# Optimization experiments

Measured on AMD Instinct MI355X. Metric: run time of the kernel, lower is better.

## Reference

```python
import jax, jax.numpy as jnp
import numpy as np

B, T, L, V, C = 4096, 200, 8, 64, 16
N_BERN = 32        # first 32 vars are bernoulli (sigmoid link), last 32 poisson (exp link)
LINPRED_MAX = 20.0


def setup_inputs() -> dict:
    key = jax.random.key(0)
    ks = jax.random.split(key, 6)
    return {
        "epsilon": jax.random.normal(ks[0], (B, T, L), dtype=jnp.float32),
        "u": jax.random.normal(ks[1], (B, 1, V), dtype=jnp.float32),
        "x": jax.random.normal(ks[2], (B, T, C), dtype=jnp.float32),
        # learned parameters (per VARGLLVM.__init__)
        "A": jax.random.normal(ks[3], (L, L), dtype=jnp.float32) * 0.1,
        "logvar_z1": jnp.zeros((L,), dtype=jnp.float32),
        "beta0": jnp.zeros((L,), dtype=jnp.float32),   # VAR1_intercept (frozen zeros)
        "beta1": jnp.zeros((L,), dtype=jnp.float32),   # VAR1_slope (frozen zeros)
        "intercepts": jnp.zeros((V,), dtype=jnp.float32),
        "wz": jax.random.normal(ks[4], (L, V), dtype=jnp.float32) * 0.1,
        "wx": jax.random.normal(ks[5], (C, V), dtype=jnp.float32) * 0.1,
        "logvar_u": jnp.zeros((V,), dtype=jnp.float32),
    }


def _var1(epsilon, A, logvar_z1, beta0, beta1):
    """z_1 = eps_1 * sqrt(exp(logvar_z1)); z_t = z_{t-1} @ A + beta0 + beta1*t + eps_t."""
    z0 = epsilon[:, 0, :] * jnp.exp(0.5 * logvar_z1)          # (B, L)
    eps_rest = jnp.swapaxes(epsilon[:, 1:, :], 0, 1)          # (T-1, B, L)
    ts = jnp.arange(1, epsilon.shape[1], dtype=epsilon.dtype)  # (T-1,)

    def step(z_prev, inp):
        eps_t, t = inp
        z_t = z_prev @ A + beta0 + beta1 * t + eps_t
        return z_t, z_t

    _, zs = jax.lax.scan(step, z0, (eps_rest, ts))            # (T-1, B, L)
    z = jnp.concatenate([z0[None], zs], axis=0)               # (T, B, L)
    return jnp.swapaxes(z, 0, 1)                              # (B, T, L)


def reference(epsilon, u, x, A, logvar_z1, beta0, beta1, intercepts, wz, wx, logvar_u):
    z = _var1(epsilon, A, logvar_z1, beta0, beta1)            # (B, T, L)
    linpar = (intercepts[None, None, :]
              + x @ wx                                        # (B, T, V)
              + z @ wz                                        # (B, T, V)
              + u * jnp.exp(0.5 * logvar_u)[None, None, :])   # broadcast (B, 1, V)
    linpar = jnp.clip(linpar, -LINPRED_MAX, LINPRED_MAX)
    is_bern = jnp.arange(V) < N_BERN                          # (V,) link selector
    condmean = jnp.where(is_bern, jax.nn.sigmoid(linpar), jnp.exp(linpar))
    return linpar, condmean
```

## Files before the change

kernel.cpp:

```cpp
#include <hip/hip_runtime.h>
#include <hip/hip_bf16.h>

#define BB 4096
#define TT 200
#define LL 8
#define VV 64
#define CC 16
#define NBERN 32
#define CLIP 20.0f
#define TC 25
#define NCH (TT / TC)
#define TOTW (BB * NCH)
#define WPB 4
#define LBLK (TOTW / WPB)
#define XF4 (TC * CC / 4)
#define ZF4 (TC * LL / 4)
#define BUF4T (XF4 + ZF4)
#define SEGT 25

__global__ __launch_bounds__(64) void var1_v4(
    const float* __restrict__ eps,
    const float* __restrict__ A,
    const float* __restrict__ logvar_z1,
    const float* __restrict__ beta0,
    const float* __restrict__ beta1,
    float* __restrict__ zout)
{
    const int tid = threadIdx.x;
    const int bl  = tid >> 3;
    const int s   = tid & 7;
    const int b   = blockIdx.x * 8 + bl;

    __shared__ float Mb[2][64];
    __shared__ float Pw8[64];
    __shared__ float P[64];
    __shared__ float zendS[8][8][8];
    __shared__ float initS[8][8][8];

    const int pi = tid >> 3, pj = tid & 7;
    Mb[0][tid] = A[pi * 8 + pj];
    __syncthreads();
    float v;
    v = 0.f;
#pragma unroll
    for (int l = 0; l < 8; ++l) v = fmaf(Mb[0][pi*8+l], Mb[0][l*8+pj], v);
    Mb[1][tid] = v; __syncthreads();
    v = 0.f;
#pragma unroll
    for (int l = 0; l < 8; ++l) v = fmaf(Mb[1][pi*8+l], Mb[1][l*8+pj], v);
    Mb[0][tid] = v; __syncthreads();
    v = 0.f;
#pragma unroll
    for (int l = 0; l < 8; ++l) v = fmaf(Mb[0][pi*8+l], Mb[0][l*8+pj], v);
    Mb[1][tid] = v; Pw8[tid] = v; __syncthreads();
    v = 0.f;
#pragma unroll
    for (int l = 0; l < 8; ++l) v = fmaf(Mb[1][pi*8+l], Mb[1][l*8+pj], v);
    Mb[0][tid] = v; __syncthreads();
    v = 0.f;
#pragma unroll
    for (int l = 0; l < 8; ++l) v = fmaf(Mb[0][pi*8+l], Pw8[l*8+pj], v);
    Mb[1][tid] = v; __syncthreads();
    v = 0.f;
#pragma unroll
    for (int l = 0; l < 8; ++l) v = fmaf(Mb[1][pi*8+l], A[l*8+pj], v);
    P[tid] = v; __syncthreads();

    float Am[8][8], B0[8], B1[8], SL[8];
#pragma unroll
    for (int l = 0; l < 8; ++l)
#pragma unroll
        for (int jj = 0; jj < 8; ++jj) Am[l][jj] = A[l * 8 + jj];
#pragma unroll
    for (int jj = 0; jj < 8; ++jj) {
        B0[jj] = beta0[jj];
        B1[jj] = beta1[jj];
        SL[jj] = __expf(0.5f * logvar_z1[jj]);
    }

    const float* myeps = eps + ((size_t)b * TT + s * SEGT) * LL;
    const int k0 = (s == 0) ? 1 : 0;

    float z[8];
#pragma unroll
    for (int jj = 0; jj < 8; ++jj) z[jj] = 0.f;
    if (s == 0) {
#pragma unroll
        for (int jj = 0; jj < 8; ++jj) z[jj] = myeps[jj] * SL[jj];
    }
#pragma unroll 5
    for (int k = k0; k < SEGT; ++k) {
        const int t = s * SEGT + k;
        const float4 e0 = *(const float4*)(myeps + k * 8);
        const float4 e1 = *(const float4*)(myeps + k * 8 + 4);
        const float ef[8] = {e0.x, e0.y, e0.z, e0.w, e1.x, e1.y, e1.z, e1.w};
        const float tf = (float)t;
        float zn[8];
#pragma unroll
        for (int jj = 0; jj < 8; ++jj) {
            float a = fmaf(B1[jj], tf, B0[jj]) + ef[jj];
#pragma unroll
            for (int l = 0; l < 8; ++l) a = fmaf(z[l], Am[l][jj], a);
            zn[jj] = a;
        }
#pragma unroll
        for (int jj = 0; jj < 8; ++jj) z[jj] = zn[jj];
    }
#pragma unroll
    for (int jj = 0; jj < 8; ++jj) zendS[bl][s][jj] = z[jj];
    __syncthreads();

    if (s == 0) {
        float E[8];
#pragma unroll
        for (int jj = 0; jj < 8; ++jj) E[jj] = zendS[bl][0][jj];
        for (int ss = 1; ss < 8; ++ss) {
#pragma unroll
            for (int jj = 0; jj < 8; ++jj) initS[bl][ss][jj] = E[jj];
            float En[8];
#pragma unroll
            for (int jj = 0; jj < 8; ++jj) {
                float c = 0.f;
#pragma unroll
                for (int l = 0; l < 8; ++l) c = fmaf(E[l], P[l * 8 + jj], c);
                En[jj] = zendS[bl][ss][jj] + c;
            }
#pragma unroll
            for (int jj = 0; jj < 8; ++jj) E[jj] = En[jj];
        }
    }
    __syncthreads();

    float* zb = zout + ((size_t)b * TT + s * SEGT) * LL;
    if (s == 0) {
#pragma unroll
        for (int jj = 0; jj < 8; ++jj) z[jj] = myeps[jj] * SL[jj];
        *(float4*)(zb)     = make_float4(z[0], z[1], z[2], z[3]);
        *(float4*)(zb + 4) = make_float4(z[4], z[5], z[6], z[7]);
    } else {
#pragma unroll
        for (int jj = 0; jj < 8; ++jj) z[jj] = initS[bl][s][jj];
    }
#pragma unroll 5
    for (int k = k0; k < SEGT; ++k) {
        const int t = s * SEGT + k;
        const float4 e0 = *(const float4*)(myeps + k * 8);
        const float4 e1 = *(const float4*)(myeps + k * 8 + 4);
        const float ef[8] = {e0.x, e0.y, e0.z, e0.w, e1.x, e1.y, e1.z, e1.w};
        const float tf = (float)t;
        float zn[8];
#pragma unroll
        for (int jj = 0; jj < 8; ++jj) {
            float a = fmaf(B1[jj], tf, B0[jj]) + ef[jj];
#pragma unroll
            for (int l = 0; l < 8; ++l) a = fmaf(z[l], Am[l][jj], a);
            zn[jj] = a;
        }
#pragma unroll
        for (int jj = 0; jj < 8; ++jj) z[jj] = zn[jj];
        *(float4*)(zb + (size_t)k * 8)     = make_float4(z[0], z[1], z[2], z[3]);
        *(float4*)(zb + (size_t)k * 8 + 4) = make_float4(z[4], z[5], z[6], z[7]);
    }
}

__global__ __launch_bounds__(256) void link_nt(
    const float* __restrict__ z,
    const float* __restrict__ u,
    const float* __restrict__ x,
    const float* __restrict__ intercepts,
    const float* __restrict__ wz,
    const float* __restrict__ wx,
    const float* __restrict__ logvar_u,
    float* __restrict__ lp_out,
    float* __restrict__ cm_out)
{
    const int w    = threadIdx.x >> 6;
    const int lane = threadIdx.x & 63;
    const int gw   = blockIdx.x * WPB + w;
    const int b    = gw >> 3;
    const int t0   = (gw & 7) * TC;
    const int v    = lane;

    __shared__ __align__(16) float4 buf[WPB][BUF4T];

    float wxv[CC];
#pragma unroll
    for (int c = 0; c < CC; ++c) wxv[c] = wx[c * VV + v];
    float wzv[LL];
#pragma unroll
    for (int l = 0; l < LL; ++l) wzv[l] = wz[l * VV + v];
    const float base = intercepts[v] + u[(size_t)b * VV + v] * __expf(0.5f * logvar_u[v]);

    const float4* gx4 = (const float4*)(x + ((size_t)b * TT + t0) * CC);
    const float4* gz4 = (const float4*)(z + ((size_t)b * TT + t0) * LL);
    float4* bw = buf[w];
    {
        const int i0 = lane;
        bw[i0] = (i0 < XF4) ? gx4[i0] : gz4[i0 - XF4];
        const int i1 = lane + 64;
        bw[i1] = (i1 < XF4) ? gx4[i1] : gz4[i1 - XF4];
        const int i2 = lane + 128;
        if (i2 < BUF4T) bw[i2] = gz4[i2 - XF4];
    }

    const float4* xs4 = bw;
    const float4* zs4 = bw + XF4;

    float* lp = lp_out + ((size_t)b * TT + t0) * VV + v;
    float* cm = cm_out + ((size_t)b * TT + t0) * VV + v;

    float4 cx0 = xs4[0], cx1 = xs4[1], cx2 = xs4[2], cx3 = xs4[3];
    float4 cz0 = zs4[0], cz1 = zs4[1];

    for (int tt = 0; tt < TC; ++tt) {
        float4 nx0, nx1, nx2, nx3, nz0, nz1;
        if (tt + 1 < TC) {
            nx0 = xs4[(tt + 1) * 4 + 0]; nx1 = xs4[(tt + 1) * 4 + 1];
            nx2 = xs4[(tt + 1) * 4 + 2]; nx3 = xs4[(tt + 1) * 4 + 3];
            nz0 = zs4[(tt + 1) * 2 + 0]; nz1 = zs4[(tt + 1) * 2 + 1];
        }

        float a0 = base, a1 = 0.f, a2 = 0.f, a3 = 0.f;
        a0 = fmaf(cx0.x, wxv[0],  a0); a0 = fmaf(cx0.y, wxv[1],  a0);
        a0 = fmaf(cx0.z, wxv[2],  a0); a0 = fmaf(cx0.w, wxv[3],  a0);
        a1 = fmaf(cx1.x, wxv[4],  a1); a1 = fmaf(cx1.y, wxv[5],  a1);
        a1 = fmaf(cx1.z, wxv[6],  a1); a1 = fmaf(cx1.w, wxv[7],  a1);
        a2 = fmaf(cx2.x, wxv[8],  a2); a2 = fmaf(cx2.y, wxv[9],  a2);
        a2 = fmaf(cx2.z, wxv[10], a2); a2 = fmaf(cx2.w, wxv[11], a2);
        a3 = fmaf(cx3.x, wxv[12], a3); a3 = fmaf(cx3.y, wxv[13], a3);
        a3 = fmaf(cx3.z, wxv[14], a3); a3 = fmaf(cx3.w, wxv[15], a3);
        a0 = fmaf(cz0.x, wzv[0],  a0); a0 = fmaf(cz0.y, wzv[1],  a0);
        a1 = fmaf(cz0.z, wzv[2],  a1); a1 = fmaf(cz0.w, wzv[3],  a1);
        a2 = fmaf(cz1.x, wzv[4],  a2); a2 = fmaf(cz1.y, wzv[5],  a2);
        a3 = fmaf(cz1.z, wzv[6],  a3); a3 = fmaf(cz1.w, wzv[7],  a3);

        float acc = (a0 + a1) + (a2 + a3);
        acc = fminf(fmaxf(acc, -CLIP), CLIP);
        const float cmv = (v < NBERN) ? (1.0f / (1.0f + __expf(-acc)))
                                      : __expf(acc);
        __builtin_nontemporal_store(acc, lp + (size_t)tt * VV);
        __builtin_nontemporal_store(cmv, cm + (size_t)tt * VV);

        cx0 = nx0; cx1 = nx1; cx2 = nx2; cx3 = nx3;
        cz0 = nz0; cz1 = nz1;
    }
}

__global__ __launch_bounds__(256) void vargllvm_fused(
    const float* __restrict__ eps, const float* __restrict__ u,
    const float* __restrict__ x, const float* __restrict__ A,
    const float* __restrict__ logvar_z1, const float* __restrict__ beta0,
    const float* __restrict__ beta1, const float* __restrict__ intercepts,
    const float* __restrict__ wz, const float* __restrict__ wx,
    const float* __restrict__ logvar_u,
    float* __restrict__ linpar_out, float* __restrict__ condmean_out)
{
    const int wave = threadIdx.x >> 6;
    const int lane = threadIdx.x & 63;
    const int b    = blockIdx.x * 4 + wave;
    const int v    = lane;

    float wxv[CC];
#pragma unroll
    for (int c = 0; c < CC; ++c) wxv[c] = wx[c * VV + v];
    float wzv[LL];
#pragma unroll
    for (int l = 0; l < LL; ++l) wzv[l] = wz[l * VV + v];
    const float base = intercepts[v] + u[(size_t)b * VV + v] * __expf(0.5f * logvar_u[v]);

    float Ar[LL][LL];
#pragma unroll
    for (int l = 0; l < LL; ++l)
#pragma unroll
        for (int j = 0; j < LL; ++j) Ar[l][j] = A[l * LL + j];
    float b0[LL], b1[LL];
#pragma unroll
    for (int j = 0; j < LL; ++j) { b0[j] = beta0[j]; b1[j] = beta1[j]; }

    const float* epsb = eps + (size_t)b * TT * LL;
    const float* xb   = x   + (size_t)b * TT * CC;
    float* lp = linpar_out   + (size_t)b * TT * VV + v;
    float* cm = condmean_out + (size_t)b * TT * VV + v;

    float zv[LL];
#pragma unroll
    for (int j = 0; j < LL; ++j) zv[j] = epsb[j] * __expf(0.5f * logvar_z1[j]);

    for (int t = 0; t < TT; ++t) {
        if (t > 0) {
            float zn[LL];
            const float tf = (float)t;
#pragma unroll
            for (int j = 0; j < LL; ++j) {
                float a = fmaf(b1[j], tf, b0[j]) + epsb[t * LL + j];
#pragma unroll
                for (int l = 0; l < LL; ++l) a = fmaf(zv[l], Ar[l][j], a);
                zn[j] = a;
            }
#pragma unroll
            for (int j = 0; j < LL; ++j) zv[j] = zn[j];
        }
        float acc = base;
#pragma unroll
        for (int c = 0; c < CC; ++c) acc = fmaf(xb[t * CC + c], wxv[c], acc);
#pragma unroll
        for (int l = 0; l < LL; ++l) acc = fmaf(zv[l], wzv[l], acc);
        acc = fminf(fmaxf(acc, -CLIP), CLIP);
        float cmv = (v < NBERN) ? (1.0f / (1.0f + __expf(-acc))) : __expf(acc);
        lp[(size_t)t * VV] = acc;
        cm[(size_t)t * VV] = cmv;
    }
}

extern "C" void kernel_launch(void* const* d_in, const int* in_sizes, int n_in,
                              void* d_out, int out_size, void* d_ws, size_t ws_size,
                              hipStream_t stream) {
    const float* eps        = (const float*)d_in[0];
    const float* u          = (const float*)d_in[1];
    const float* x          = (const float*)d_in[2];
    const float* A          = (const float*)d_in[3];
    const float* logvar_z1  = (const float*)d_in[4];
    const float* beta0      = (const float*)d_in[5];
    const float* beta1      = (const float*)d_in[6];
    const float* intercepts = (const float*)d_in[7];
    const float* wz         = (const float*)d_in[8];
    const float* wx         = (const float*)d_in[9];
    const float* logvar_u   = (const float*)d_in[10];

    float* linpar   = (float*)d_out;
    float* condmean = (float*)d_out + (size_t)BB * TT * VV;

    const size_t z_bytes = (size_t)BB * TT * LL * sizeof(float);
    if (ws_size >= z_bytes) {
        float* zws = (float*)d_ws;
        hipLaunchKernelGGL(var1_v4, dim3(BB / 8), dim3(64), 0, stream,
                           eps, A, logvar_z1, beta0, beta1, zws);
        hipLaunchKernelGGL(link_nt, dim3(LBLK), dim3(256), 0, stream,
                           zws, u, x, intercepts, wz, wx, logvar_u, linpar, condmean);
    } else {
        hipLaunchKernelGGL(vargllvm_fused, dim3(BB / 4), dim3(256), 0, stream,
                           eps, u, x, A, logvar_z1, beta0, beta1,
                           intercepts, wz, wx, logvar_u, linpar, condmean);
    }
}
```

Before: 103.6 us.

## Write only chunk boundary states and recompute VAR1 trajectory inside link kernel

```diff
diff --git a/kernel.cpp b/kernel.cpp
--- a/kernel.cpp
+++ b/kernel.cpp
@@ -14,17 +14,16 @@
 #define WPB 4
 #define LBLK (TOTW / WPB)
 #define XF4 (TC * CC / 4)
-#define ZF4 (TC * LL / 4)
-#define BUF4T (XF4 + ZF4)
+#define EF4 (TC * LL / 4)
 #define SEGT 25
 
-__global__ __launch_bounds__(64) void var1_v4(
+__global__ __launch_bounds__(64) void var1_b(
     const float* __restrict__ eps,
     const float* __restrict__ A,
     const float* __restrict__ logvar_z1,
     const float* __restrict__ beta0,
     const float* __restrict__ beta1,
-    float* __restrict__ zout)
+    float* __restrict__ Eout)
 {
     const int tid = threadIdx.x;
     const int bl  = tid >> 3;
@@ -111,6 +110,8 @@
     __syncthreads();
 
     if (s == 0) {
+#pragma unroll
+        for (int jj = 0; jj < 8; ++jj) initS[bl][0][jj] = myeps[jj] * SL[jj];
         float E[8];
 #pragma unroll
         for (int jj = 0; jj < 8; ++jj) E[jj] = zendS[bl][0][jj];
@@ -131,42 +132,21 @@
     }
     __syncthreads();
 
-    float* zb = zout + ((size_t)b * TT + s * SEGT) * LL;
-    if (s == 0) {
-#pragma unroll
-        for (int jj = 0; jj < 8; ++jj) z[jj] = myeps[jj] * SL[jj];
-        *(float4*)(zb)     = make_float4(z[0], z[1], z[2], z[3]);
-        *(float4*)(zb + 4) = make_float4(z[4], z[5], z[6], z[7]);
-    } else {
-#pragma unroll
-        for (int jj = 0; jj < 8; ++jj) z[jj] = initS[bl][s][jj];
-    }
-#pragma unroll 5
-    for (int k = k0; k < SEGT; ++k) {
-        const int t = s * SEGT + k;
-        const float4 e0 = *(const float4*)(myeps + k * 8);
-        const float4 e1 = *(const float4*)(myeps + k * 8 + 4);
-        const float ef[8] = {e0.x, e0.y, e0.z, e0.w, e1.x, e1.y, e1.z, e1.w};
-        const float tf = (float)t;
-        float zn[8];
-#pragma unroll
-        for (int jj = 0; jj < 8; ++jj) {
-            float a = fmaf(B1[jj], tf, B0[jj]) + ef[jj];
-#pragma unroll
-            for (int l = 0; l < 8; ++l) a = fmaf(z[l], Am[l][jj], a);
-            zn[jj] = a;
-        }
-#pragma unroll
-        for (int jj = 0; jj < 8; ++jj) z[jj] = zn[jj];
-        *(float4*)(zb + (size_t)k * 8)     = make_float4(z[0], z[1], z[2], z[3]);
-        *(float4*)(zb + (size_t)k * 8 + 4) = make_float4(z[4], z[5], z[6], z[7]);
-    }
+    float* eo = Eout + (((size_t)b * NCH) + s) * 8;
+    *(float4*)(eo)     = make_float4(initS[bl][s][0], initS[bl][s][1],
+                                     initS[bl][s][2], initS[bl][s][3]);
+    *(float4*)(eo + 4) = make_float4(initS[bl][s][4], initS[bl][s][5],
+                                     initS[bl][s][6], initS[bl][s][7]);
 }
 
-__global__ __launch_bounds__(256) void link_nt(
-    const float* __restrict__ z,
+__global__ __launch_bounds__(256) void link_f(
+    const float* __restrict__ Eb,
+    const float* __restrict__ eps,
     const float* __restrict__ u,
     const float* __restrict__ x,
+    const float* __restrict__ A,
+    const float* __restrict__ beta0,
+    const float* __restrict__ beta1,
     const float* __restrict__ intercepts,
     const float* __restrict__ wz,
     const float* __restrict__ wx,
@@ -178,33 +158,60 @@
     const int lane = threadIdx.x & 63;
     const int gw   = blockIdx.x * WPB + w;
     const int b    = gw >> 3;
-    const int t0   = (gw & 7) * TC;
+    const int c    = gw & 7;
+    const int t0   = c * TC;
     const int v    = lane;
 
-    __shared__ __align__(16) float4 buf[WPB][BUF4T];
+    __shared__ __align__(16) float4 xs[WPB][XF4];
+    __shared__ __align__(16) float  epsS[WPB][TC * LL];
+    __shared__ __align__(16) float  zbS[WPB][TC * LL];
 
     float wxv[CC];
 #pragma unroll
-    for (int c = 0; c < CC; ++c) wxv[c] = wx[c * VV + v];
+    for (int cc = 0; cc < CC; ++cc) wxv[cc] = wx[cc * VV + v];
     float wzv[LL];
 #pragma unroll
     for (int l = 0; l < LL; ++l) wzv[l] = wz[l * VV + v];
     const float base = intercepts[v] + u[(size_t)b * VV + v] * __expf(0.5f * logvar_u[v]);
 
-    const float4* gx4 = (const float4*)(x + ((size_t)b * TT + t0) * CC);
-    const float4* gz4 = (const float4*)(z + ((size_t)b * TT + t0) * LL);
-    float4* bw = buf[w];
+    const float4* gx4 = (const float4*)(x   + ((size_t)b * TT + t0) * CC);
+    const float4* ge4 = (const float4*)(eps + ((size_t)b * TT + t0) * LL);
+    float4* ew = (float4*)epsS[w];
     {
         const int i0 = lane;
-        bw[i0] = (i0 < XF4) ? gx4[i0] : gz4[i0 - XF4];
+        if (i0 < XF4) xs[w][i0] = gx4[i0]; else ew[i0 - XF4] = ge4[i0 - XF4];
         const int i1 = lane + 64;
-        bw[i1] = (i1 < XF4) ? gx4[i1] : gz4[i1 - XF4];
+        if (i1 < XF4) xs[w][i1] = gx4[i1]; else ew[i1 - XF4] = ge4[i1 - XF4];
         const int i2 = lane + 128;
-        if (i2 < BUF4T) bw[i2] = gz4[i2 - XF4];
-    }
-
-    const float4* xs4 = bw;
-    const float4* zs4 = bw + XF4;
+        if (i2 < XF4 + EF4) ew[i2 - XF4] = ge4[i2 - XF4];
+    }
+
+    {
+        const int j = lane & 7;
+        float Ac[LL];
+#pragma unroll
+        for (int l = 0; l < LL; ++l) Ac[l] = A[l * LL + j];
+        const float b0j = beta0[j];
+        const float b1j = beta1[j];
+        float zj = 0.f;
+        if (lane < 8) {
+            zj = Eb[(((size_t)b * NCH) + c) * 8 + j];
+            int kstart = 0;
+            if (c == 0) { zbS[w][j] = zj; kstart = 1; }
+            for (int k = kstart; k < TC; ++k) {
+                const int t = t0 + k;
+                float a = fmaf(b1j, (float)t, b0j) + epsS[w][k * 8 + j];
+#pragma unroll
+                for (int l = 0; l < LL; ++l)
+                    a = fmaf(__shfl(zj, l), Ac[l], a);
+                zj = a;
+                zbS[w][k * 8 + j] = zj;
+            }
+        }
+    }
+
+    const float4* xs4 = xs[w];
+    const float4* zs4 = (const float4*)zbS[w];
 
     float* lp = lp_out + ((size_t)b * TT + t0) * VV + v;
     float* cm = cm_out + ((size_t)b * TT + t0) * VV + v;
@@ -262,7 +269,7 @@
 
     float wxv[CC];
 #pragma unroll
-    for (int c = 0; c < CC; ++c) wxv[c] = wx[c * VV + v];
+    for (int cc = 0; cc < CC; ++cc) wxv[cc] = wx[cc * VV + v];
     float wzv[LL];
 #pragma unroll
     for (int l = 0; l < LL; ++l) wzv[l] = wz[l * VV + v];
@@ -302,7 +309,7 @@
         }
         float acc = base;
 #pragma unroll
-        for (int c = 0; c < CC; ++c) acc = fmaf(xb[t * CC + c], wxv[c], acc);
+        for (int cc = 0; cc < CC; ++cc) acc = fmaf(xb[t * CC + cc], wxv[cc], acc);
 #pragma unroll
         for (int l = 0; l < LL; ++l) acc = fmaf(zv[l], wzv[l], acc);
         acc = fminf(fmaxf(acc, -CLIP), CLIP);
@@ -330,13 +337,14 @@
     float* linpar   = (float*)d_out;
     float* condmean = (float*)d_out + (size_t)BB * TT * VV;
 
-    const size_t z_bytes = (size_t)BB * TT * LL * sizeof(float);
-    if (ws_size >= z_bytes) {
-        float* zws = (float*)d_ws;
-        hipLaunchKernelGGL(var1_v4, dim3(BB / 8), dim3(64), 0, stream,
-                           eps, A, logvar_z1, beta0, beta1, zws);
-        hipLaunchKernelGGL(link_nt, dim3(LBLK), dim3(256), 0, stream,
-                           zws, u, x, intercepts, wz, wx, logvar_u, linpar, condmean);
+    const size_t e_bytes = (size_t)BB * NCH * 8 * sizeof(float);
+    if (ws_size >= e_bytes) {
+        float* Ews = (float*)d_ws;
+        hipLaunchKernelGGL(var1_b, dim3(BB / 8), dim3(64), 0, stream,
+                           eps, A, logvar_z1, beta0, beta1, Ews);
+        hipLaunchKernelGGL(link_f, dim3(LBLK), dim3(256), 0, stream,
+                           Ews, eps, u, x, A, beta0, beta1,
+                           intercepts, wz, wx, logvar_u, linpar, condmean);
     } else {
         hipLaunchKernelGGL(vargllvm_fused, dim3(BB / 4), dim3(256), 0, stream,
                            eps, u, x, A, logvar_z1, beta0, beta1,
```

After: 133.6 us. +28.9%, slower.

## Fuse VAR1 scan and link computation into one kernel via shared-memory z

Applied to the files above, without the earlier changes.

```diff
diff --git a/kernel.cpp b/kernel.cpp
--- a/kernel.cpp
+++ b/kernel.cpp
@@ -10,163 +10,17 @@
 #define CLIP 20.0f
 #define TC 25
 #define NCH (TT / TC)
-#define TOTW (BB * NCH)
-#define WPB 4
-#define LBLK (TOTW / WPB)
-#define XF4 (TC * CC / 4)
-#define ZF4 (TC * LL / 4)
-#define BUF4T (XF4 + ZF4)
 #define SEGT 25
-
-__global__ __launch_bounds__(64) void var1_v4(
+#define XF4C (TC * CC / 4)
+
+__global__ __launch_bounds__(256) void vargllvm_one(
     const float* __restrict__ eps,
+    const float* __restrict__ u,
+    const float* __restrict__ x,
     const float* __restrict__ A,
     const float* __restrict__ logvar_z1,
     const float* __restrict__ beta0,
     const float* __restrict__ beta1,
-    float* __restrict__ zout)
-{
-    const int tid = threadIdx.x;
-    const int bl  = tid >> 3;
-    const int s   = tid & 7;
-    const int b   = blockIdx.x * 8 + bl;
-
-    __shared__ float Mb[2][64];
-    __shared__ float Pw8[64];
-    __shared__ float P[64];
-    __shared__ float zendS[8][8][8];
-    __shared__ float initS[8][8][8];
-
-    const int pi = tid >> 3, pj = tid & 7;
-    Mb[0][tid] = A[pi * 8 + pj];
-    __syncthreads();
-    float v;
-    v = 0.f;
-#pragma unroll
-    for (int l = 0; l < 8; ++l) v = fmaf(Mb[0][pi*8+l], Mb[0][l*8+pj], v);
-    Mb[1][tid] = v; __syncthreads();
-    v = 0.f;
-#pragma unroll
-    for (int l = 0; l < 8; ++l) v = fmaf(Mb[1][pi*8+l], Mb[1][l*8+pj], v);
-    Mb[0][tid] = v; __syncthreads();
-    v = 0.f;
-#pragma unroll
-    for (int l = 0; l < 8; ++l) v = fmaf(Mb[0][pi*8+l], Mb[0][l*8+pj], v);
-    Mb[1][tid] = v; Pw8[tid] = v; __syncthreads();
-    v = 0.f;
-#pragma unroll
-    for (int l = 0; l < 8; ++l) v = fmaf(Mb[1][pi*8+l], Mb[1][l*8+pj], v);
-    Mb[0][tid] = v; __syncthreads();
-    v = 0.f;
-#pragma unroll
-    for (int l = 0; l < 8; ++l) v = fmaf(Mb[0][pi*8+l], Pw8[l*8+pj], v);
-    Mb[1][tid] = v; __syncthreads();
-    v = 0.f;
-#pragma unroll
-    for (int l = 0; l < 8; ++l) v = fmaf(Mb[1][pi*8+l], A[l*8+pj], v);
-    P[tid] = v; __syncthreads();
-
-    float Am[8][8], B0[8], B1[8], SL[8];
-#pragma unroll
-    for (int l = 0; l < 8; ++l)
-#pragma unroll
-        for (int jj = 0; jj < 8; ++jj) Am[l][jj] = A[l * 8 + jj];
-#pragma unroll
-    for (int jj = 0; jj < 8; ++jj) {
-        B0[jj] = beta0[jj];
-        B1[jj] = beta1[jj];
-        SL[jj] = __expf(0.5f * logvar_z1[jj]);
-    }
-
-    const float* myeps = eps + ((size_t)b * TT + s * SEGT) * LL;
-    const int k0 = (s == 0) ? 1 : 0;
-
-    float z[8];
-#pragma unroll
-    for (int jj = 0; jj < 8; ++jj) z[jj] = 0.f;
-    if (s == 0) {
-#pragma unroll
-        for (int jj = 0; jj < 8; ++jj) z[jj] = myeps[jj] * SL[jj];
-    }
-#pragma unroll 5
-    for (int k = k0; k < SEGT; ++k) {
-        const int t = s * SEGT + k;
-        const float4 e0 = *(const float4*)(myeps + k * 8);
-        const float4 e1 = *(const float4*)(myeps + k * 8 + 4);
-        const float ef[8] = {e0.x, e0.y, e0.z, e0.w, e1.x, e1.y, e1.z, e1.w};
-        const float tf = (float)t;
-        float zn[8];
-#pragma unroll
-        for (int jj = 0; jj < 8; ++jj) {
-            float a = fmaf(B1[jj], tf, B0[jj]) + ef[jj];
-#pragma unroll
-            for (int l = 0; l < 8; ++l) a = fmaf(z[l], Am[l][jj], a);
-            zn[jj] = a;
-        }
-#pragma unroll
-        for (int jj = 0; jj < 8; ++jj) z[jj] = zn[jj];
-    }
-#pragma unroll
-    for (int jj = 0; jj < 8; ++jj) zendS[bl][s][jj] = z[jj];
-    __syncthreads();
-
-    if (s == 0) {
-        float E[8];
-#pragma unroll
-        for (int jj = 0; jj < 8; ++jj) E[jj] = zendS[bl][0][jj];
-        for (int ss = 1; ss < 8; ++ss) {
-#pragma unroll
-            for (int jj = 0; jj < 8; ++jj) initS[bl][ss][jj] = E[jj];
-            float En[8];
-#pragma unroll
-            for (int jj = 0; jj < 8; ++jj) {
-                float c = 0.f;
-#pragma unroll
-                for (int l = 0; l < 8; ++l) c = fmaf(E[l], P[l * 8 + jj], c);
-                En[jj] = zendS[bl][ss][jj] + c;
-            }
-#pragma unroll
-            for (int jj = 0; jj < 8; ++jj) E[jj] = En[jj];
-        }
-    }
-    __syncthreads();
-
-    float* zb = zout + ((size_t)b * TT + s * SEGT) * LL;
-    if (s == 0) {
-#pragma unroll
-        for (int jj = 0; jj < 8; ++jj) z[jj] = myeps[jj] * SL[jj];
-        *(float4*)(zb)     = make_float4(z[0], z[1], z[2], z[3]);
-        *(float4*)(zb + 4) = make_float4(z[4], z[5], z[6], z[7]);
-    } else {
-#pragma unroll
-        for (int jj = 0; jj < 8; ++jj) z[jj] = initS[bl][s][jj];
-    }
-#pragma unroll 5
-    for (int k = k0; k < SEGT; ++k) {
-        const int t = s * SEGT + k;
-        const float4 e0 = *(const float4*)(myeps + k * 8);
-        const float4 e1 = *(const float4*)(myeps + k * 8 + 4);
-        const float ef[8] = {e0.x, e0.y, e0.z, e0.w, e1.x, e1.y, e1.z, e1.w};
-        const float tf = (float)t;
-        float zn[8];
-#pragma unroll
-        for (int jj = 0; jj < 8; ++jj) {
-            float a = fmaf(B1[jj], tf, B0[jj]) + ef[jj];
-#pragma unroll
-            for (int l = 0; l < 8; ++l) a = fmaf(z[l], Am[l][jj], a);
-            zn[jj] = a;
-        }
-#pragma unroll
-        for (int jj = 0; jj < 8; ++jj) z[jj] = zn[jj];
-        *(float4*)(zb + (size_t)k * 8)     = make_float4(z[0], z[1], z[2], z[3]);
-        *(float4*)(zb + (size_t)k * 8 + 4) = make_float4(z[4], z[5], z[6], z[7]);
-    }
-}
-
-__global__ __launch_bounds__(256) void link_nt(
-    const float* __restrict__ z,
-    const float* __restrict__ u,
-    const float* __restrict__ x,
     const float* __restrict__ intercepts,
     const float* __restrict__ wz,
     const float* __restrict__ wx,
@@ -174,141 +28,244 @@
     float* __restrict__ lp_out,
     float* __restrict__ cm_out)
 {
-    const int w    = threadIdx.x >> 6;
-    const int lane = threadIdx.x & 63;
-    const int gw   = blockIdx.x * WPB + w;
-    const int b    = gw >> 3;
-    const int t0   = (gw & 7) * TC;
+    const int tid = threadIdx.x;
+    const int b0  = blockIdx.x * 4;
+
+    __shared__ float Mb[2][64];
+    __shared__ float Pw8[64];
+    __shared__ float P[64];
+    __shared__ float zendS[4][8][8];
+    __shared__ float initS[4][8][8];
+    __shared__ __align__(16) float  zS[4][TT * LL];
+    __shared__ __align__(16) float4 xs[4][XF4C];
+
+    {
+        const int pi = (tid & 63) >> 3, pj = tid & 7;
+        if (tid < 64) Mb[0][tid] = A[pi * 8 + pj];
+        __syncthreads();
+        if (tid < 64) {
+            float v = 0.f;
+#pragma unroll
+            for (int l = 0; l < 8; ++l) v = fmaf(Mb[0][pi*8+l], Mb[0][l*8+pj], v);
+            Mb[1][tid] = v;
+        }
+        __syncthreads();
+        if (tid < 64) {
+            float v = 0.f;
+#pragma unroll
+            for (int l = 0; l < 8; ++l) v = fmaf(Mb[1][pi*8+l], Mb[1][l*8+pj], v);
+            Mb[0][tid] = v;
+        }
+        __syncthreads();
+        if (tid < 64) {
+            float v = 0.f;
+#pragma unroll
+            for (int l = 0; l < 8; ++l) v = fmaf(Mb[0][pi*8+l], Mb[0][l*8+pj], v);
+            Mb[1][tid] = v; Pw8[tid] = v;
+        }
+        __syncthreads();
+        if (tid < 64) {
+            float v = 0.f;
+#pragma unroll
+            for (int l = 0; l < 8; ++l) v = fmaf(Mb[1][pi*8+l], Mb[1][l*8+pj], v);
+            Mb[0][tid] = v;
+        }
+        __syncthreads();
+        if (tid < 64) {
+            float v = 0.f;
+#pragma unroll
+            for (int l = 0; l < 8; ++l) v = fmaf(Mb[0][pi*8+l], Pw8[l*8+pj], v);
+            Mb[1][tid] = v;
+        }
+        __syncthreads();
+        if (tid < 64) {
+            float v = 0.f;
+#pragma unroll
+            for (int l = 0; l < 8; ++l) v = fmaf(Mb[1][pi*8+l], A[l*8+pj], v);
+            P[tid] = v;
+        }
+        __syncthreads();
+    }
+
+    if (tid < 32) {
+        const int bl = tid >> 3, s = tid & 7;
+        const int b  = b0 + bl;
+        float Am[8][8], B0r[8], B1r[8], SLr[8];
+#pragma unroll
+        for (int l = 0; l < 8; ++l)
+#pragma unroll
+            for (int jj = 0; jj < 8; ++jj) Am[l][jj] = A[l * 8 + jj];
+#pragma unroll
+        for (int jj = 0; jj < 8; ++jj) {
+            B0r[jj] = beta0[jj];
+            B1r[jj] = beta1[jj];
+            SLr[jj] = __expf(0.5f * logvar_z1[jj]);
+        }
+        const float* myeps = eps + ((size_t)b * TT + s * SEGT) * LL;
+        const int k0 = (s == 0) ? 1 : 0;
+
+        float z[8];
+#pragma unroll
+        for (int jj = 0; jj < 8; ++jj) z[jj] = 0.f;
+        if (s == 0) {
+#pragma unroll
+            for (int jj = 0; jj < 8; ++jj) {
+                z[jj] = myeps[jj] * SLr[jj];
+                initS[bl][0][jj] = z[jj];
+            }
+        }
+#pragma unroll 5
+        for (int k = k0; k < SEGT; ++k) {
+            const int t = s * SEGT + k;
+            const float4 e0 = *(const float4*)(myeps + k * 8);
+            const float4 e1 = *(const float4*)(myeps + k * 8 + 4);
+            const float ef[8] = {e0.x, e0.y, e0.z, e0.w, e1.x, e1.y, e1.z, e1.w};
+            const float tf = (float)t;
+            float zn[8];
+#pragma unroll
+            for (int jj = 0; jj < 8; ++jj) {
+                float a = fmaf(B1r[jj], tf, B0r[jj]) + ef[jj];
+#pragma unroll
+                for (int l = 0; l < 8; ++l) a = fmaf(z[l], Am[l][jj], a);
+                zn[jj] = a;
+            }
+#pragma unroll
+            for (int jj = 0; jj < 8; ++jj) z[jj] = zn[jj];
+        }
+#pragma unroll
+        for (int jj = 0; jj < 8; ++jj) zendS[bl][s][jj] = z[jj];
+    }
+    __syncthreads();
+
+    if (tid < 4) {
+        const int bl = tid;
+        float E[8];
+#pragma unroll
+        for (int jj = 0; jj < 8; ++jj) E[jj] = zendS[bl][0][jj];
+        for (int ss = 1; ss < 8; ++ss) {
+#pragma unroll
+            for (int jj = 0; jj < 8; ++jj) initS[bl][ss][jj] = E[jj];
+            float En[8];
+#pragma unroll
+            for (int jj = 0; jj < 8; ++jj) {
+                float c = 0.f;
+#pragma unroll
+                for (int l = 0; l < 8; ++l) c = fmaf(E[l], P[l * 8 + jj], c);
+                En[jj] = zendS[bl][ss][jj] + c;
+            }
+#pragma unroll
+            for (int jj = 0; jj < 8; ++jj) E[jj] = En[jj];
+        }
+    }
+    __syncthreads();
+
+    if (tid < 32) {
+        const int bl = tid >> 3, s = tid & 7;
+        const int b  = b0 + bl;
+        float Am[8][8], B0r[8], B1r[8];
+#pragma unroll
+        for (int l = 0; l < 8; ++l)
+#pragma unroll
+            for (int jj = 0; jj < 8; ++jj) Am[l][jj] = A[l * 8 + jj];
+#pragma unroll
+        for (int jj = 0; jj < 8; ++jj) {
+            B0r[jj] = beta0[jj];
+            B1r[jj] = beta1[jj];
+        }
+        const float* myeps = eps + ((size_t)b * TT + s * SEGT) * LL;
+        const int k0 = (s == 0) ? 1 : 0;
+
+        float z[8];
+#pragma unroll
+        for (int jj = 0; jj < 8; ++jj) z[jj] = initS[bl][s][jj];
+        if (s == 0) {
+            *(float4*)(&zS[bl][0]) = make_float4(z[0], z[1], z[2], z[3]);
+            *(float4*)(&zS[bl][4]) = make_float4(z[4], z[5], z[6], z[7]);
+        }
+#pragma unroll 5
+        for (int k = k0; k < SEGT; ++k) {
+            const int t = s * SEGT + k;
+            const float4 e0 = *(const float4*)(myeps + k * 8);
+            const float4 e1 = *(const float4*)(myeps + k * 8 + 4);
+            const float ef[8] = {e0.x, e0.y, e0.z, e0.w, e1.x, e1.y, e1.z, e1.w};
+            const float tf = (float)t;
+            float zn[8];
+#pragma unroll
+            for (int jj = 0; jj < 8; ++jj) {
+                float a = fmaf(B1r[jj], tf, B0r[jj]) + ef[jj];
+#pragma unroll
+                for (int l = 0; l < 8; ++l) a = fmaf(z[l], Am[l][jj], a);
+                zn[jj] = a;
+            }
+#pragma unroll
+            for (int jj = 0; jj < 8; ++jj) z[jj] = zn[jj];
+            float* zrow = &zS[bl][(size_t)t * 8];
+            *(float4*)(zrow)     = make_float4(z[0], z[1], z[2], z[3]);
+            *(float4*)(zrow + 4) = make_float4(z[4], z[5], z[6], z[7]);
+        }
+    }
+    __syncthreads();
+
+    const int w    = tid >> 6;
+    const int lane = tid & 63;
     const int v    = lane;
-
-    __shared__ __align__(16) float4 buf[WPB][BUF4T];
+    const int b    = b0 + w;
 
     float wxv[CC];
 #pragma unroll
-    for (int c = 0; c < CC; ++c) wxv[c] = wx[c * VV + v];
+    for (int cc = 0; cc < CC; ++cc) wxv[cc] = wx[cc * VV + v];
     float wzv[LL];
 #pragma unroll
     for (int l = 0; l < LL; ++l) wzv[l] = wz[l * VV + v];
     const float base = intercepts[v] + u[(size_t)b * VV + v] * __expf(0.5f * logvar_u[v]);
 
-    const float4* gx4 = (const float4*)(x + ((size_t)b * TT + t0) * CC);
-    const float4* gz4 = (const float4*)(z + ((size_t)b * TT + t0) * LL);
-    float4* bw = buf[w];
-    {
-        const int i0 = lane;
-        bw[i0] = (i0 < XF4) ? gx4[i0] : gz4[i0 - XF4];
-        const int i1 = lane + 64;
-        bw[i1] = (i1 < XF4) ? gx4[i1] : gz4[i1 - XF4];
-        const int i2 = lane + 128;
-        if (i2 < BUF4T) bw[i2] = gz4[i2 - XF4];
-    }
-
-    const float4* xs4 = bw;
-    const float4* zs4 = bw + XF4;
-
-    float* lp = lp_out + ((size_t)b * TT + t0) * VV + v;
-    float* cm = cm_out + ((size_t)b * TT + t0) * VV + v;
-
-    float4 cx0 = xs4[0], cx1 = xs4[1], cx2 = xs4[2], cx3 = xs4[3];
-    float4 cz0 = zs4[0], cz1 = zs4[1];
-
-    for (int tt = 0; tt < TC; ++tt) {
-        float4 nx0, nx1, nx2, nx3, nz0, nz1;
-        if (tt + 1 < TC) {
-            nx0 = xs4[(tt + 1) * 4 + 0]; nx1 = xs4[(tt + 1) * 4 + 1];
-            nx2 = xs4[(tt + 1) * 4 + 2]; nx3 = xs4[(tt + 1) * 4 + 3];
-            nz0 = zs4[(tt + 1) * 2 + 0]; nz1 = zs4[(tt + 1) * 2 + 1];
-        }
-
-        float a0 = base, a1 = 0.f, a2 = 0.f, a3 = 0.f;
-        a0 = fmaf(cx0.x, wxv[0],  a0); a0 = fmaf(cx0.y, wxv[1],  a0);
-        a0 = fmaf(cx0.z, wxv[2],  a0); a0 = fmaf(cx0.w, wxv[3],  a0);
-        a1 = fmaf(cx1.x, wxv[4],  a1); a1 = fmaf(cx1.y, wxv[5],  a1);
-        a1 = fmaf(cx1.z, wxv[6],  a1); a1 = fmaf(cx1.w, wxv[7],  a1);
-        a2 = fmaf(cx2.x, wxv[8],  a2); a2 = fmaf(cx2.y, wxv[9],  a2);
-        a2 = fmaf(cx2.z, wxv[10], a2); a2 = fmaf(cx2.w, wxv[11], a2);
-        a3 = fmaf(cx3.x, wxv[12], a3); a3 = fmaf(cx3.y, wxv[13], a3);
-        a3 = fmaf(cx3.z, wxv[14], a3); a3 = fmaf(cx3.w, wxv[15], a3);
-        a0 = fmaf(cz0.x, wzv[0],  a0); a0 = fmaf(cz0.y, wzv[1],  a0);
-        a1 = fmaf(cz0.z, wzv[2],  a1); a1 = fmaf(cz0.w, wzv[3],  a1);
-        a2 = fmaf(cz1.x, wzv[4],  a2); a2 = fmaf(cz1.y, wzv[5],  a2);
-        a3 = fmaf(cz1.z, wzv[6],  a3); a3 = fmaf(cz1.w, wzv[7],  a3);
-
-        float acc = (a0 + a1) + (a2 + a3);
-        acc = fminf(fmaxf(acc, -CLIP), CLIP);
-        const float cmv = (v < NBERN) ? (1.0f / (1.0f + __expf(-acc)))
-                                      : __expf(acc);
-        __builtin_nontemporal_store(acc, lp + (size_t)tt * VV);
-        __builtin_nontemporal_store(cmv, cm + (size_t)tt * VV);
-
-        cx0 = nx0; cx1 = nx1; cx2 = nx2; cx3 = nx3;
-        cz0 = nz0; cz1 = nz1;
-    }
-}
-
-__global__ __launch_bounds__(256) void vargllvm_fused(
-    const float* __restrict__ eps, const float* __restrict__ u,
-    const float* __restrict__ x, const float* __restrict__ A,
-    const float* __restrict__ logvar_z1, const float* __restrict__ beta0,
-    const float* __restrict__ beta1, const float* __restrict__ intercepts,
-    const float* __restrict__ wz, const float* __restrict__ wx,
-    const float* __restrict__ logvar_u,
-    float* __restrict__ linpar_out, float* __restrict__ condmean_out)
-{
-    const int wave = threadIdx.x >> 6;
-    const int lane = threadIdx.x & 63;
-    const int b    = blockIdx.x * 4 + wave;
-    const int v    = lane;
-
-    float wxv[CC];
-#pragma unroll
-    for (int c = 0; c < CC; ++c) wxv[c] = wx[c * VV + v];
-    float wzv[LL];
-#pragma unroll
-    for (int l = 0; l < LL; ++l) wzv[l] = wz[l * VV + v];
-    const float base = intercepts[v] + u[(size_t)b * VV + v] * __expf(0.5f * logvar_u[v]);
-
-    float Ar[LL][LL];
-#pragma unroll
-    for (int l = 0; l < LL; ++l)
-#pragma unroll
-        for (int j = 0; j < LL; ++j) Ar[l][j] = A[l * LL + j];
-    float b0[LL], b1[LL];
-#pragma unroll
-    for (int j = 0; j < LL; ++j) { b0[j] = beta0[j]; b1[j] = beta1[j]; }
-
-    const float* epsb = eps + (size_t)b * TT * LL;
-    const float* xb   = x   + (size_t)b * TT * CC;
-    float* lp = linpar_out   + (size_t)b * TT * VV + v;
-    float* cm = condmean_out + (size_t)b * TT * VV + v;
-
-    float zv[LL];
-#pragma unroll
-    for (int j = 0; j < LL; ++j) zv[j] = epsb[j] * __expf(0.5f * logvar_z1[j]);
-
-    for (int t = 0; t < TT; ++t) {
-        if (t > 0) {
-            float zn[LL];
-            const float tf = (float)t;
-#pragma unroll
-            for (int j = 0; j < LL; ++j) {
-                float a = fmaf(b1[j], tf, b0[j]) + epsb[t * LL + j];
-#pragma unroll
-                for (int l = 0; l < LL; ++l) a = fmaf(zv[l], Ar[l][j], a);
-                zn[j] = a;
-            }
-#pragma unroll
-            for (int j = 0; j < LL; ++j) zv[j] = zn[j];
-        }
-        float acc = base;
-#pragma unroll
-        for (int c = 0; c < CC; ++c) acc = fmaf(xb[t * CC + c], wxv[c], acc);
-#pragma unroll
-        for (int l = 0; l < LL; ++l) acc = fmaf(zv[l], wzv[l], acc);
-        acc = fminf(fmaxf(acc, -CLIP), CLIP);
-        float cmv = (v < NBERN) ? (1.0f / (1.0f + __expf(-acc))) : __expf(acc);
-        lp[(size_t)t * VV] = acc;
-        cm[(size_t)t * VV] = cmv;
+    float* lp = lp_out + (size_t)b * TT * VV + v;
+    float* cm = cm_out + (size_t)b * TT * VV + v;
+
+    for (int cc = 0; cc < NCH; ++cc) {
+        const int t0 = cc * TC;
+        const float4* gx4 = (const float4*)(x + ((size_t)b * TT + t0) * CC);
+        xs[w][lane] = gx4[lane];
+        if (lane + 64 < XF4C) xs[w][lane + 64] = gx4[lane + 64];
+
+        const float4* xs4 = xs[w];
+        const float4* zs4 = (const float4*)&zS[w][(size_t)t0 * 8];
+
+        float4 cx0 = xs4[0], cx1 = xs4[1], cx2 = xs4[2], cx3 = xs4[3];
+        float4 cz0 = zs4[0], cz1 = zs4[1];
+
+        for (int tt = 0; tt < TC; ++tt) {
+            float4 nx0, nx1, nx2, nx3, nz0, nz1;
+            if (tt + 1 < TC) {
+                nx0 = xs4[(tt + 1) * 4 + 0]; nx1 = xs4[(tt + 1) * 4 + 1];
+                nx2 = xs4[(tt + 1) * 4 + 2]; nx3 = xs4[(tt + 1) * 4 + 3];
+                nz0 = zs4[(tt + 1) * 2 + 0]; nz1 = zs4[(tt + 1) * 2 + 1];
+            }
+
+            float a0 = base, a1 = 0.f, a2 = 0.f, a3 = 0.f;
+            a0 = fmaf(cx0.x, wxv[0],  a0); a0 = fmaf(cx0.y, wxv[1],  a0);
+            a0 = fmaf(cx0.z, wxv[2],  a0); a0 = fmaf(cx0.w, wxv[3],  a0);
+            a1 = fmaf(cx1.x, wxv[4],  a1); a1 = fmaf(cx1.y, wxv[5],  a1);
+            a1 = fmaf(cx1.z, wxv[6],  a1); a1 = fmaf(cx1.w, wxv[7],  a1);
+            a2 = fmaf(cx2.x, wxv[8],  a2); a2 = fmaf(cx2.y, wxv[9],  a2);
+            a2 = fmaf(cx2.z, wxv[10], a2); a2 = fmaf(cx2.w, wxv[11], a2);
+            a3 = fmaf(cx3.x, wxv[12], a3); a3 = fmaf(cx3.y, wxv[13], a3);
+            a3 = fmaf(cx3.z, wxv[14], a3); a3 = fmaf(cx3.w, wxv[15], a3);
+            a0 = fmaf(cz0.x, wzv[0],  a0); a0 = fmaf(cz0.y, wzv[1],  a0);
+            a1 = fmaf(cz0.z, wzv[2],  a1); a1 = fmaf(cz0.w, wzv[3],  a1);
+            a2 = fmaf(cz1.x, wzv[4],  a2); a2 = fmaf(cz1.y, wzv[5],  a2);
+            a3 = fmaf(cz1.z, wzv[6],  a3); a3 = fmaf(cz1.w, wzv[7],  a3);
+
+            float acc = (a0 + a1) + (a2 + a3);
+            acc = fminf(fmaxf(acc, -CLIP), CLIP);
+            const float cmv = (v < NBERN) ? (1.0f / (1.0f + __expf(-acc)))
+                                          : __expf(acc);
+            __builtin_nontemporal_store(acc, lp + (size_t)(t0 + tt) * VV);
+            __builtin_nontemporal_store(cmv, cm + (size_t)(t0 + tt) * VV);
+
+            cx0 = nx0; cx1 = nx1; cx2 = nx2; cx3 = nx3;
+            cz0 = nz0; cz1 = nz1;
+        }
     }
 }
 
@@ -330,16 +287,7 @@
     float* linpar   = (float*)d_out;
     float* condmean = (float*)d_out + (size_t)BB * TT * VV;
 
-    const size_t z_bytes = (size_t)BB * TT * LL * sizeof(float);
-    if (ws_size >= z_bytes) {
-        float* zws = (float*)d_ws;
-        hipLaunchKernelGGL(var1_v4, dim3(BB / 8), dim3(64), 0, stream,
-                           eps, A, logvar_z1, beta0, beta1, zws);
-        hipLaunchKernelGGL(link_nt, dim3(LBLK), dim3(256), 0, stream,
-                           zws, u, x, intercepts, wz, wx, logvar_u, linpar, condmean);
-    } else {
-        hipLaunchKernelGGL(vargllvm_fused, dim3(BB / 4), dim3(256), 0, stream,
-                           eps, u, x, A, logvar_z1, beta0, beta1,
-                           intercepts, wz, wx, logvar_u, linpar, condmean);
-    }
+    hipLaunchKernelGGL(vargllvm_one, dim3(BB / 4), dim3(256), 0, stream,
+                       eps, u, x, A, logvar_z1, beta0, beta1,
+                       intercepts, wz, wx, logvar_u, linpar, condmean);
 }
```

Measured after the change: 117.8 us. 13.7% more time.

## Split VAR(1) scan into 20 shorter segments with 16 batches per block

Applied to the files above, without the earlier changes.

```diff
diff --git a/kernel.cpp b/kernel.cpp
--- a/kernel.cpp
+++ b/kernel.cpp
@@ -16,9 +16,13 @@
 #define XF4 (TC * CC / 4)
 #define ZF4 (TC * LL / 4)
 #define BUF4T (XF4 + ZF4)
-#define SEGT 25
-
-__global__ __launch_bounds__(64) void var1_v4(
+
+#define SEGT 10
+#define NSEG (TT / SEGT)
+#define BPB 16
+#define VTHR (BPB * NSEG)
+
+__global__ __launch_bounds__(VTHR) void var1_v5(
     const float* __restrict__ eps,
     const float* __restrict__ A,
     const float* __restrict__ logvar_z1,
@@ -27,55 +31,61 @@
     float* __restrict__ zout)
 {
     const int tid = threadIdx.x;
-    const int bl  = tid >> 3;
-    const int s   = tid & 7;
-    const int b   = blockIdx.x * 8 + bl;
+    const int bl  = tid / NSEG;
+    const int s   = tid % NSEG;
+    const int b   = blockIdx.x * BPB + bl;
 
     __shared__ float Mb[2][64];
-    __shared__ float Pw8[64];
     __shared__ float P[64];
-    __shared__ float zendS[8][8][8];
-    __shared__ float initS[8][8][8];
-
-    const int pi = tid >> 3, pj = tid & 7;
-    Mb[0][tid] = A[pi * 8 + pj];
-    __syncthreads();
-    float v;
-    v = 0.f;
-#pragma unroll
-    for (int l = 0; l < 8; ++l) v = fmaf(Mb[0][pi*8+l], Mb[0][l*8+pj], v);
-    Mb[1][tid] = v; __syncthreads();
-    v = 0.f;
-#pragma unroll
-    for (int l = 0; l < 8; ++l) v = fmaf(Mb[1][pi*8+l], Mb[1][l*8+pj], v);
-    Mb[0][tid] = v; __syncthreads();
-    v = 0.f;
-#pragma unroll
-    for (int l = 0; l < 8; ++l) v = fmaf(Mb[0][pi*8+l], Mb[0][l*8+pj], v);
-    Mb[1][tid] = v; Pw8[tid] = v; __syncthreads();
-    v = 0.f;
-#pragma unroll
-    for (int l = 0; l < 8; ++l) v = fmaf(Mb[1][pi*8+l], Mb[1][l*8+pj], v);
-    Mb[0][tid] = v; __syncthreads();
-    v = 0.f;
-#pragma unroll
-    for (int l = 0; l < 8; ++l) v = fmaf(Mb[0][pi*8+l], Pw8[l*8+pj], v);
-    Mb[1][tid] = v; __syncthreads();
-    v = 0.f;
-#pragma unroll
-    for (int l = 0; l < 8; ++l) v = fmaf(Mb[1][pi*8+l], A[l*8+pj], v);
-    P[tid] = v; __syncthreads();
-
-    float Am[8][8], B0[8], B1[8], SL[8];
+    __shared__ float zendS[BPB][NSEG][8];
+    __shared__ float initS[BPB][NSEG][8];
+
+    {
+        const int pi = (tid & 63) >> 3, pj = tid & 7;
+        if (tid < 64) Mb[0][tid] = A[pi * 8 + pj];
+        __syncthreads();
+        if (tid < 64) {
+            float v = 0.f;
+#pragma unroll
+            for (int l = 0; l < 8; ++l) v = fmaf(Mb[0][pi*8+l], Mb[0][l*8+pj], v);
+            Mb[1][tid] = v;
+        }
+        __syncthreads();
+        if (tid < 64) {
+            float v = 0.f;
+#pragma unroll
+            for (int l = 0; l < 8; ++l) v = fmaf(Mb[1][pi*8+l], Mb[1][l*8+pj], v);
+            Mb[0][tid] = v;
+        }
+        __syncthreads();
+        if (tid < 64) {
+            float v = 0.f;
+#pragma unroll
+            for (int l = 0; l < 8; ++l) v = fmaf(Mb[0][pi*8+l], Mb[0][l*8+pj], v);
+            P[tid] = v;
+        }
+        __syncthreads();
+        if (tid < 64) {
+            float v = 0.f;
+#pragma unroll
+            for (int l = 0; l < 8; ++l) v = fmaf(P[pi*8+l], Mb[1][l*8+pj], v);
+            Mb[0][tid] = v;
+        }
+        __syncthreads();
+        if (tid < 64) P[tid] = Mb[0][tid];
+        __syncthreads();
+    }
+
+    float Am[8][8], B0r[8], B1r[8], SLr[8];
 #pragma unroll
     for (int l = 0; l < 8; ++l)
 #pragma unroll
         for (int jj = 0; jj < 8; ++jj) Am[l][jj] = A[l * 8 + jj];
 #pragma unroll
     for (int jj = 0; jj < 8; ++jj) {
-        B0[jj] = beta0[jj];
-        B1[jj] = beta1[jj];
-        SL[jj] = __expf(0.5f * logvar_z1[jj]);
+        B0r[jj] = beta0[jj];
+        B1r[jj] = beta1[jj];
+        SLr[jj] = __expf(0.5f * logvar_z1[jj]);
     }
 
     const float* myeps = eps + ((size_t)b * TT + s * SEGT) * LL;
@@ -86,7 +96,10 @@
     for (int jj = 0; jj < 8; ++jj) z[jj] = 0.f;
     if (s == 0) {
 #pragma unroll
-        for (int jj = 0; jj < 8; ++jj) z[jj] = myeps[jj] * SL[jj];
+        for (int jj = 0; jj < 8; ++jj) {
+            z[jj] = myeps[jj] * SLr[jj];
+            initS[bl][0][jj] = z[jj];
+        }
     }
 #pragma unroll 5
     for (int k = k0; k < SEGT; ++k) {
@@ -98,7 +111,7 @@
         float zn[8];
 #pragma unroll
         for (int jj = 0; jj < 8; ++jj) {
-            float a = fmaf(B1[jj], tf, B0[jj]) + ef[jj];
+            float a = fmaf(B1r[jj], tf, B0r[jj]) + ef[jj];
 #pragma unroll
             for (int l = 0; l < 8; ++l) a = fmaf(z[l], Am[l][jj], a);
             zn[jj] = a;
@@ -111,10 +124,13 @@
     __syncthreads();
 
     if (s == 0) {
+        float Pr[64];
+#pragma unroll
+        for (int i = 0; i < 64; ++i) Pr[i] = P[i];
         float E[8];
 #pragma unroll
         for (int jj = 0; jj < 8; ++jj) E[jj] = zendS[bl][0][jj];
-        for (int ss = 1; ss < 8; ++ss) {
+        for (int ss = 1; ss < NSEG; ++ss) {
 #pragma unroll
             for (int jj = 0; jj < 8; ++jj) initS[bl][ss][jj] = E[jj];
             float En[8];
@@ -122,7 +138,7 @@
             for (int jj = 0; jj < 8; ++jj) {
                 float c = 0.f;
 #pragma unroll
-                for (int l = 0; l < 8; ++l) c = fmaf(E[l], P[l * 8 + jj], c);
+                for (int l = 0; l < 8; ++l) c = fmaf(E[l], Pr[l * 8 + jj], c);
                 En[jj] = zendS[bl][ss][jj] + c;
             }
 #pragma unroll
@@ -132,14 +148,11 @@
     __syncthreads();
 
     float* zb = zout + ((size_t)b * TT + s * SEGT) * LL;
+#pragma unroll
+    for (int jj = 0; jj < 8; ++jj) z[jj] = initS[bl][s][jj];
     if (s == 0) {
-#pragma unroll
-        for (int jj = 0; jj < 8; ++jj) z[jj] = myeps[jj] * SL[jj];
         *(float4*)(zb)     = make_float4(z[0], z[1], z[2], z[3]);
         *(float4*)(zb + 4) = make_float4(z[4], z[5], z[6], z[7]);
-    } else {
-#pragma unroll
-        for (int jj = 0; jj < 8; ++jj) z[jj] = initS[bl][s][jj];
     }
 #pragma unroll 5
     for (int k = k0; k < SEGT; ++k) {
@@ -151,7 +164,7 @@
         float zn[8];
 #pragma unroll
         for (int jj = 0; jj < 8; ++jj) {
-            float a = fmaf(B1[jj], tf, B0[jj]) + ef[jj];
+            float a = fmaf(B1r[jj], tf, B0r[jj]) + ef[jj];
 #pragma unroll
             for (int l = 0; l < 8; ++l) a = fmaf(z[l], Am[l][jj], a);
             zn[jj] = a;
@@ -262,7 +275,7 @@
 
     float wxv[CC];
 #pragma unroll
-    for (int c = 0; c < CC; ++c) wxv[c] = wx[c * VV + v];
+    for (int cc = 0; cc < CC; ++cc) wxv[cc] = wx[cc * VV + v];
     float wzv[LL];
 #pragma unroll
     for (int l = 0; l < LL; ++l) wzv[l] = wz[l * VV + v];
@@ -302,7 +315,7 @@
         }
         float acc = base;
 #pragma unroll
-        for (int c = 0; c < CC; ++c) acc = fmaf(xb[t * CC + c], wxv[c], acc);
+        for (int cc = 0; cc < CC; ++cc) acc = fmaf(xb[t * CC + cc], wxv[cc], acc);
 #pragma unroll
         for (int l = 0; l < LL; ++l) acc = fmaf(zv[l], wzv[l], acc);
         acc = fminf(fmaxf(acc, -CLIP), CLIP);
@@ -333,7 +346,7 @@
     const size_t z_bytes = (size_t)BB * TT * LL * sizeof(float);
     if (ws_size >= z_bytes) {
         float* zws = (float*)d_ws;
-        hipLaunchKernelGGL(var1_v4, dim3(BB / 8), dim3(64), 0, stream,
+        hipLaunchKernelGGL(var1_v5, dim3(BB / BPB), dim3(VTHR), 0, stream,
                            eps, A, logvar_z1, beta0, beta1, zws);
         hipLaunchKernelGGL(link_nt, dim3(LBLK), dim3(256), 0, stream,
                            zws, u, x, intercepts, wz, wx, logvar_u, linpar, condmean);
```

After: 112.0 us. 8.0% more time.
